# Kernel optimization log

Hardware: AMD Instinct MI355X
Metric: run time of the kernel (lower is better)

The kernel has to match this reference:

```python
import jax, jax.numpy as jnp
import numpy as np

SQRT2 = 1.4142135623730951  # ScaleCostWeight(sqrt(2)) applied to residuals
N_ITERS = 10
DAMP = 1e-8  # tiny Tikhonov for numerical safety of the 6x6 solve


def _hat(phi):
    x, y, z = phi[0], phi[1], phi[2]
    o = jnp.zeros((), phi.dtype)
    return jnp.stack([jnp.stack([o, -z, y]),
                      jnp.stack([z, o, -x]),
                      jnp.stack([-y, x, o])])


def se3_exp(xi):
    # xi: [6] = [rho (trans), phi (rot)] -> 4x4 SE3 matrix
    rho, phi = xi[:3], xi[3:]
    theta2 = jnp.sum(phi * phi)
    small = theta2 < 1e-12
    theta2s = jnp.where(small, 1.0, theta2)  # double-where for safe grads
    theta = jnp.sqrt(theta2s)
    A = jnp.where(small, 1.0, jnp.sin(theta) / theta)
    B = jnp.where(small, 0.5, (1.0 - jnp.cos(theta)) / theta2s)
    C = jnp.where(small, 1.0 / 6.0, (theta - jnp.sin(theta)) / (theta2s * theta))
    K = _hat(phi)
    K2 = K @ K
    I3 = jnp.eye(3, dtype=xi.dtype)
    R = I3 + A * K + B * K2
    V = I3 + B * K + C * K2
    t = V @ rho
    top = jnp.concatenate([R, t[:, None]], axis=1)
    bot = jnp.array([[0.0, 0.0, 0.0, 1.0]], dtype=xi.dtype)
    return jnp.concatenate([top, bot], axis=0)


def se3_inv(T):
    R = T[..., :3, :3]
    t = T[..., :3, 3:]
    Rt = jnp.swapaxes(R, -1, -2)
    top = jnp.concatenate([Rt, -(Rt @ t)], axis=-1)
    bot = jnp.broadcast_to(jnp.array([0.0, 0.0, 0.0, 1.0], T.dtype),
                           T.shape[:-2] + (1, 4))
    return jnp.concatenate([top, bot], axis=-2)


def _r_single(xi, T, src3, trg3, Wh, w):
    # residual of one batch element at local perturbation xi (retract on right)
    Tn = T @ se3_exp(xi)
    pred = Tn[:3, :3] @ src3 + Tn[:3, 3:4]          # [3, N]
    e = trg3 - pred                                  # [3, N]
    ew = jnp.einsum('nij,jn->in', Wh, e) * w         # cholesky-weighted, w: [1,N]
    return (ew * SQRT2).reshape(-1)                  # [3N]


def _forward(src4, trg4, w, T_init, inv_cov, T_s_v):
    src3 = src4[:, :3, :]
    trg3 = trg4[:, :3, :]
    # W_half = cholesky(inv_cov)^T, computed once (aux var, constant over iters)
    Wh = jnp.swapaxes(jnp.linalg.cholesky(inv_cov), -1, -2)  # [B, N, 3, 3]
    B = src4.shape[0]
    I6 = jnp.eye(6, dtype=src4.dtype)

    def step(T, _):
        xi0 = jnp.zeros((B, 6), T.dtype)
        J = jax.vmap(jax.jacfwd(_r_single), in_axes=(0, 0, 0, 0, 0, 0))(
            xi0, T, src3, trg3, Wh, w)               # [B, 3N, 6]
        r = jax.vmap(_r_single)(xi0, T, src3, trg3, Wh, w)  # [B, 3N]
        g = jnp.einsum('bri,br->bi', J, r)
        H = jnp.einsum('bri,brj->bij', J, J) + DAMP * I6
        dx = -jnp.linalg.solve(H, g[..., None])[..., 0]
        return T @ jax.vmap(se3_exp)(dx), None

    T, _ = jax.lax.scan(step, T_init, None, length=N_ITERS)
    T_sv = jnp.broadcast_to(T_s_v, (B, 4, 4))
    return se3_inv(T_sv) @ T @ T_sv


def setup_inputs() -> dict:
    key = jax.random.key(0)
    B, N = 256, 2048
    k1, k2, k3, k4, k5, k6 = jax.random.split(key, 6)
    src3 = 2.0 * jax.random.normal(k1, (B, 3, N), dtype=jnp.float32)
    # well-posed registration problem: trg = T_true * src + noise
    T_true = jax.vmap(se3_exp)(0.3 * jax.random.normal(k2, (B, 6), dtype=jnp.float32))
    trg3 = (jnp.einsum('bij,bjn->bin', T_true[:, :3, :3], src3)
            + T_true[:, :3, 3:4]
            + 0.01 * jax.random.normal(k3, (B, 3, N), dtype=jnp.float32))
    ones = jnp.ones((B, 1, N), dtype=jnp.float32)
    keypoints_3D_src = jnp.concatenate([src3, ones], axis=1)
    keypoints_3D_trg = jnp.concatenate([trg3, ones], axis=1)
    weights = jax.random.uniform(k4, (B, 1, N), dtype=jnp.float32,
                                 minval=0.1, maxval=1.0)
    A = 0.3 * jax.random.normal(k5, (B, N, 3, 3), dtype=jnp.float32)
    inv_cov_weights = A @ jnp.swapaxes(A, -1, -2) + jnp.eye(3, dtype=jnp.float32)
    T_trg_src_init = jax.vmap(se3_exp)(
        0.05 * jax.random.normal(k6, (B, 6), dtype=jnp.float32))
    T_s_v = se3_exp(jnp.array([0.1, -0.2, 0.3, 0.2, -0.1, 0.15], dtype=jnp.float32))
    return {"keypoints_3D_src": keypoints_3D_src,
            "keypoints_3D_trg": keypoints_3D_trg,
            "weights": weights,
            "T_trg_src_init": T_trg_src_init,
            "inv_cov_weights": inv_cov_weights,
            "T_s_v": T_s_v}


def reference(keypoints_3D_src, keypoints_3D_trg, weights, T_trg_src_init,
              inv_cov_weights, T_s_v):
    return _forward(keypoints_3D_src, keypoints_3D_trg, weights,
                    T_trg_src_init, inv_cov_weights, T_s_v)
```

## Files before the change

### kernel.cpp

```cpp
#include <hip/hip_runtime.h>
#include <math.h>

#define NPTS   2048
#define BD1    256
#define SPLIT  2
#define PPB    (NPTS / SPLIT)
#define PPT    (PPB / BD1)
#define NMOM   72
#define NITERS 10
#define DAMPF  1e-8f

__launch_bounds__(BD1, 1)
__global__ void moments_kernel(const float* __restrict__ src4,
                               const float* __restrict__ trg4,
                               const float* __restrict__ wts,
                               const float* __restrict__ icov,
                               float* __restrict__ mom, int B)
{
    const int b   = blockIdx.x >> 1;
    const int s   = blockIdx.x & 1;
    const int tid = threadIdx.x;

    const float* srcb = src4 + (size_t)b * 4 * NPTS;
    const float* trgb = trg4 + (size_t)b * 4 * NPTS;
    const float* wb   = wts  + (size_t)b * NPTS;
    const float* cb   = icov + (size_t)b * NPTS * 9;

    float acc[NMOM];
    #pragma unroll
    for (int k = 0; k < NMOM; ++k) acc[k] = 0.0f;

    #pragma unroll 2
    for (int kk = 0; kk < PPT; ++kk) {
        int n = s * PPB + kk * BD1 + tid;
        float sx = srcb[n], sy = srcb[NPTS + n], sz = srcb[2 * NPTS + n];
        float gx = trgb[n], gy = trgb[NPTS + n], gz = trgb[2 * NPTS + n];
        float w  = wb[n];
        const float* c = cb + (size_t)n * 9;
        float w2 = 2.0f * w * w;
        float W[6];
        W[0] = w2 * c[0];
        W[1] = w2 * c[3];
        W[2] = w2 * c[6];
        W[3] = w2 * c[4];
        W[4] = w2 * c[7];
        W[5] = w2 * c[8];

        float hx = W[0] * gx + W[1] * gy + W[2] * gz;
        float hy = W[1] * gx + W[3] * gy + W[4] * gz;
        float hz = W[2] * gx + W[4] * gy + W[5] * gz;

        float sv[3] = { sx, sy, sz };
        float hv[3] = { hx, hy, hz };
        float ss[6] = { sx*sx, sx*sy, sx*sz, sy*sy, sy*sz, sz*sz };

        #pragma unroll
        for (int ij = 0; ij < 6; ++ij) {
            acc[ij] += W[ij];
            #pragma unroll
            for (int c2 = 0; c2 < 3; ++c2) acc[6 + ij * 3 + c2] += W[ij] * sv[c2];
            #pragma unroll
            for (int cd = 0; cd < 6; ++cd) acc[24 + ij * 6 + cd] += W[ij] * ss[cd];
        }
        acc[60] += hx; acc[61] += hy; acc[62] += hz;
        #pragma unroll
        for (int c2 = 0; c2 < 3; ++c2)
            #pragma unroll
            for (int i = 0; i < 3; ++i) acc[63 + c2 * 3 + i] += sv[c2] * hv[i];
    }

    __shared__ float lds[36][BD1 + 1];
    #pragma unroll
    for (int h = 0; h < 2; ++h) {
        if (h) __syncthreads();
        #pragma unroll
        for (int k = 0; k < 36; ++k) lds[k][tid] = acc[h * 36 + k];
        __syncthreads();
        if (tid < 36) {
            const float* row = lds[tid];
            float s0 = 0.f, s1 = 0.f, s2 = 0.f, s3 = 0.f;
            #pragma unroll 8
            for (int j = 0; j < BD1; j += 4) {
                s0 += row[j]; s1 += row[j + 1]; s2 += row[j + 2]; s3 += row[j + 3];
            }
            mom[((size_t)s * NMOM + h * 36 + tid) * B + b] = (s0 + s1) + (s2 + s3);
        }
    }
}

__launch_bounds__(64, 1)
__global__ void solve_kernel(const float* __restrict__ mom,
                             const float* __restrict__ Tinit,
                             const float* __restrict__ Tsv,
                             float* __restrict__ out, int B)
{
    const int b = blockIdx.x * 64 + threadIdx.x;
    if (b >= B) return;

    float m[NMOM];
    #pragma unroll
    for (int k = 0; k < NMOM; ++k)
        m[k] = mom[k * B + b] + mom[(NMOM + k) * B + b];

    float Rm[3][3], tv[3];
    #pragma unroll
    for (int i = 0; i < 3; ++i) {
        #pragma unroll
        for (int j = 0; j < 3; ++j) Rm[i][j] = Tinit[b * 16 + i * 4 + j];
        tv[i] = Tinit[b * 16 + i * 4 + 3];
    }

    const int SY[3][3] = { {0,1,2}, {1,3,4}, {2,4,5} };

    for (int it = 0; it < NITERS; ++it) {
        float C1[6][3];
        #pragma unroll
        for (int ij = 0; ij < 6; ++ij) {
            float a0 = m[6 + ij * 3 + 0], a1 = m[6 + ij * 3 + 1], a2 = m[6 + ij * 3 + 2];
            #pragma unroll
            for (int a = 0; a < 3; ++a)
                C1[ij][a] = Rm[a][0] * a0 + Rm[a][1] * a1 + Rm[a][2] * a2;
        }
        float SM[3][3], SWp[3];
        #pragma unroll
        for (int i = 0; i < 3; ++i) {
            SM[i][0] = C1[SY[i][1]][2] - C1[SY[i][2]][1];
            SM[i][1] = C1[SY[i][2]][0] - C1[SY[i][0]][2];
            SM[i][2] = C1[SY[i][0]][1] - C1[SY[i][1]][0];
            SWp[i]   = C1[SY[i][0]][0] + C1[SY[i][1]][1] + C1[SY[i][2]][2];
        }
        float P2[6][6];
        #pragma unroll
        for (int ij = 0; ij < 6; ++ij) {
            float S00 = m[24 + ij * 6 + 0], S01 = m[24 + ij * 6 + 1], S02 = m[24 + ij * 6 + 2];
            float S11 = m[24 + ij * 6 + 3], S12 = m[24 + ij * 6 + 4], S22 = m[24 + ij * 6 + 5];
            float U[3][3];
            #pragma unroll
            for (int a = 0; a < 3; ++a) {
                U[a][0] = Rm[a][0] * S00 + Rm[a][1] * S01 + Rm[a][2] * S02;
                U[a][1] = Rm[a][0] * S01 + Rm[a][1] * S11 + Rm[a][2] * S12;
                U[a][2] = Rm[a][0] * S02 + Rm[a][1] * S12 + Rm[a][2] * S22;
            }
            P2[0][ij] = U[0][0]*Rm[0][0] + U[0][1]*Rm[0][1] + U[0][2]*Rm[0][2];
            P2[1][ij] = U[0][0]*Rm[1][0] + U[0][1]*Rm[1][1] + U[0][2]*Rm[1][2];
            P2[2][ij] = U[0][0]*Rm[2][0] + U[0][1]*Rm[2][1] + U[0][2]*Rm[2][2];
            P2[3][ij] = U[1][0]*Rm[1][0] + U[1][1]*Rm[1][1] + U[1][2]*Rm[1][2];
            P2[4][ij] = U[1][0]*Rm[2][0] + U[1][1]*Rm[2][1] + U[1][2]*Rm[2][2];
            P2[5][ij] = U[2][0]*Rm[2][0] + U[2][1]*Rm[2][1] + U[2][2]*Rm[2][2];
        }
        float SN00 = -P2[5][3] + 2.f * P2[4][4] - P2[3][5];
        float SN01 = -P2[2][4] + P2[5][1] + P2[1][5] - P2[4][2];
        float SN02 = -P2[4][1] + P2[2][3] + P2[3][2] - P2[1][4];
        float SN11 =  2.f * P2[2][2] - P2[5][0] - P2[0][5];
        float SN12 =  P2[4][0] - P2[2][1] - P2[1][2] + P2[0][4];
        float SN22 = -P2[3][0] + 2.f * P2[1][1] - P2[0][3];

        float SWt0 = m[0]*tv[0] + m[1]*tv[1] + m[2]*tv[2];
        float SWt1 = m[1]*tv[0] + m[3]*tv[1] + m[4]*tv[2];
        float SWt2 = m[2]*tv[0] + m[4]*tv[1] + m[5]*tv[2];
        float Su[3] = { m[60] - SWp[0] - SWt0,
                        m[61] - SWp[1] - SWt1,
                        m[62] - SWp[2] - SWt2 };

        float G[3][3];
        #pragma unroll
        for (int a = 0; a < 3; ++a)
            #pragma unroll
            for (int bb = 0; bb < 3; ++bb)
                G[a][bb] = Rm[a][0]*m[63 + 0 + bb] + Rm[a][1]*m[63 + 3 + bb] + Rm[a][2]*m[63 + 6 + bb];
        float ch[3] = { G[1][2] - G[2][1], G[2][0] - G[0][2], G[0][1] - G[1][0] };
        float pw[3];
        pw[0] = P2[1][2] + P2[3][4] + P2[4][5] - P2[2][1] - P2[4][3] - P2[5][4];
        pw[1] = P2[2][0] + P2[4][1] + P2[5][2] - P2[0][2] - P2[1][4] - P2[2][5];
        pw[2] = P2[0][1] + P2[1][3] + P2[2][4] - P2[1][0] - P2[3][1] - P2[4][2];
        float Sq[3];
        #pragma unroll
        for (int i = 0; i < 3; ++i)
            Sq[i] = ch[i] - pw[i] + SM[0][i]*tv[0] + SM[1][i]*tv[1] + SM[2][i]*tv[2];

        float Hm[6][6];
        Hm[0][0] = m[0]; Hm[0][1] = m[1]; Hm[0][2] = m[2];
        Hm[1][1] = m[3]; Hm[1][2] = m[4]; Hm[2][2] = m[5];
        #pragma unroll
        for (int i = 0; i < 3; ++i) {
            Hm[i][3] = -SM[i][0]; Hm[i][4] = -SM[i][1]; Hm[i][5] = -SM[i][2];
        }
        Hm[3][3] = -SN00; Hm[3][4] = -SN01; Hm[3][5] = -SN02;
        Hm[4][4] = -SN11; Hm[4][5] = -SN12; Hm[5][5] = -SN22;
        #pragma unroll
        for (int i = 0; i < 6; ++i) {
            Hm[i][i] += DAMPF;
            #pragma unroll
            for (int j = 0; j < 6; ++j)
                if (j < i) Hm[i][j] = Hm[j][i];
        }
        float rhs[6] = { Su[0], Su[1], Su[2], Sq[0], Sq[1], Sq[2] };

        float L[6][6];
        #pragma unroll
        for (int i = 0; i < 6; ++i) {
            #pragma unroll
            for (int j = 0; j < 6; ++j) {
                if (j > i) continue;
                float sum = Hm[i][j];
                #pragma unroll
                for (int k2 = 0; k2 < 6; ++k2)
                    if (k2 < j) sum -= L[i][k2] * L[j][k2];
                if (i == j) L[i][i] = sqrtf(sum);
                else        L[i][j] = sum / L[j][j];
            }
        }
        float z[6];
        #pragma unroll
        for (int i = 0; i < 6; ++i) {
            float sum = rhs[i];
            #pragma unroll
            for (int k2 = 0; k2 < 6; ++k2)
                if (k2 < i) sum -= L[i][k2] * z[k2];
            z[i] = sum / L[i][i];
        }
        float y[6];
        #pragma unroll
        for (int i = 5; i >= 0; --i) {
            float sum = z[i];
            #pragma unroll
            for (int k2 = 0; k2 < 6; ++k2)
                if (k2 > i) sum -= L[k2][i] * y[k2];
            y[i] = sum / L[i][i];
        }

        float drx = Rm[0][0]*y[0] + Rm[1][0]*y[1] + Rm[2][0]*y[2];
        float dry = Rm[0][1]*y[0] + Rm[1][1]*y[1] + Rm[2][1]*y[2];
        float drz = Rm[0][2]*y[0] + Rm[1][2]*y[1] + Rm[2][2]*y[2];
        float dpx = Rm[0][0]*y[3] + Rm[1][0]*y[4] + Rm[2][0]*y[5];
        float dpy = Rm[0][1]*y[3] + Rm[1][1]*y[4] + Rm[2][1]*y[5];
        float dpz = Rm[0][2]*y[3] + Rm[1][2]*y[4] + Rm[2][2]*y[5];

        float th2  = dpx*dpx + dpy*dpy + dpz*dpz;
        bool  sm   = th2 < 1e-12f;
        float th2s = sm ? 1.0f : th2;
        float th   = sqrtf(th2s);
        float sth  = sinf(th), cth = cosf(th);
        float Ae = sm ? 1.0f : sth / th;
        float Be = sm ? 0.5f : (1.0f - cth) / th2s;
        float Ce = sm ? (1.0f / 6.0f) : (th - sth) / (th2s * th);
        float Rd00 = 1.0f + Be * (dpx*dpx - th2);
        float Rd01 = -Ae * dpz + Be * dpx * dpy;
        float Rd02 =  Ae * dpy + Be * dpx * dpz;
        float Rd10 =  Ae * dpz + Be * dpx * dpy;
        float Rd11 = 1.0f + Be * (dpy*dpy - th2);
        float Rd12 = -Ae * dpx + Be * dpy * dpz;
        float Rd20 = -Ae * dpy + Be * dpx * dpz;
        float Rd21 =  Ae * dpx + Be * dpy * dpz;
        float Rd22 = 1.0f + Be * (dpz*dpz - th2);
        float V00 = 1.0f + Ce * (dpx*dpx - th2);
        float V01 = -Be * dpz + Ce * dpx * dpy;
        float V02 =  Be * dpy + Ce * dpx * dpz;
        float V10 =  Be * dpz + Ce * dpx * dpy;
        float V11 = 1.0f + Ce * (dpy*dpy - th2);
        float V12 = -Be * dpx + Ce * dpy * dpz;
        float V20 = -Be * dpy + Ce * dpx * dpz;
        float V21 =  Be * dpx + Ce * dpy * dpz;
        float V22 = 1.0f + Ce * (dpz*dpz - th2);
        float tdx = V00 * drx + V01 * dry + V02 * drz;
        float tdy = V10 * drx + V11 * dry + V12 * drz;
        float tdz = V20 * drx + V21 * dry + V22 * drz;

        float nR[3][3];
        nR[0][0] = Rm[0][0]*Rd00 + Rm[0][1]*Rd10 + Rm[0][2]*Rd20;
        nR[0][1] = Rm[0][0]*Rd01 + Rm[0][1]*Rd11 + Rm[0][2]*Rd21;
        nR[0][2] = Rm[0][0]*Rd02 + Rm[0][1]*Rd12 + Rm[0][2]*Rd22;
        nR[1][0] = Rm[1][0]*Rd00 + Rm[1][1]*Rd10 + Rm[1][2]*Rd20;
        nR[1][1] = Rm[1][0]*Rd01 + Rm[1][1]*Rd11 + Rm[1][2]*Rd21;
        nR[1][2] = Rm[1][0]*Rd02 + Rm[1][1]*Rd12 + Rm[1][2]*Rd22;
        nR[2][0] = Rm[2][0]*Rd00 + Rm[2][1]*Rd10 + Rm[2][2]*Rd20;
        nR[2][1] = Rm[2][0]*Rd01 + Rm[2][1]*Rd11 + Rm[2][2]*Rd21;
        nR[2][2] = Rm[2][0]*Rd02 + Rm[2][1]*Rd12 + Rm[2][2]*Rd22;
        float ntx = Rm[0][0]*tdx + Rm[0][1]*tdy + Rm[0][2]*tdz + tv[0];
        float nty = Rm[1][0]*tdx + Rm[1][1]*tdy + Rm[1][2]*tdz + tv[1];
        float ntz = Rm[2][0]*tdx + Rm[2][1]*tdy + Rm[2][2]*tdz + tv[2];
        #pragma unroll
        for (int i = 0; i < 3; ++i)
            #pragma unroll
            for (int j = 0; j < 3; ++j) Rm[i][j] = nR[i][j];
        tv[0] = ntx; tv[1] = nty; tv[2] = ntz;
    }

    {
        float R00 = Rm[0][0], R01 = Rm[0][1], R02 = Rm[0][2];
        float R10 = Rm[1][0], R11 = Rm[1][1], R12 = Rm[1][2];
        float R20 = Rm[2][0], R21 = Rm[2][1], R22 = Rm[2][2];
        float tx = tv[0], ty = tv[1], tz = tv[2];

        float Rv00 = Tsv[0], Rv01 = Tsv[1], Rv02 = Tsv[2],  tvx = Tsv[3];
        float Rv10 = Tsv[4], Rv11 = Tsv[5], Rv12 = Tsv[6],  tvy = Tsv[7];
        float Rv20 = Tsv[8], Rv21 = Tsv[9], Rv22 = Tsv[10], tvz = Tsv[11];

        float P00 = R00*Rv00 + R01*Rv10 + R02*Rv20;
        float P01 = R00*Rv01 + R01*Rv11 + R02*Rv21;
        float P02 = R00*Rv02 + R01*Rv12 + R02*Rv22;
        float P10 = R10*Rv00 + R11*Rv10 + R12*Rv20;
        float P11 = R10*Rv01 + R11*Rv11 + R12*Rv21;
        float P12 = R10*Rv02 + R11*Rv12 + R12*Rv22;
        float P20 = R20*Rv00 + R21*Rv10 + R22*Rv20;
        float P21 = R20*Rv01 + R21*Rv11 + R22*Rv21;
        float P22 = R20*Rv02 + R21*Rv12 + R22*Rv22;
        float Ptx = R00*tvx + R01*tvy + R02*tvz + tx;
        float Pty = R10*tvx + R11*tvy + R12*tvz + ty;
        float Ptz = R20*tvx + R21*tvy + R22*tvz + tz;

        float ex = Ptx - tvx, ey = Pty - tvy, ez = Ptz - tvz;
        float* o = out + (size_t)b * 16;
        o[0]  = Rv00*P00 + Rv10*P10 + Rv20*P20;
        o[1]  = Rv00*P01 + Rv10*P11 + Rv20*P21;
        o[2]  = Rv00*P02 + Rv10*P12 + Rv20*P22;
        o[3]  = Rv00*ex  + Rv10*ey  + Rv20*ez;
        o[4]  = Rv01*P00 + Rv11*P10 + Rv21*P20;
        o[5]  = Rv01*P01 + Rv11*P11 + Rv21*P21;
        o[6]  = Rv01*P02 + Rv11*P12 + Rv21*P22;
        o[7]  = Rv01*ex  + Rv11*ey  + Rv21*ez;
        o[8]  = Rv02*P00 + Rv12*P10 + Rv22*P20;
        o[9]  = Rv02*P01 + Rv12*P11 + Rv22*P21;
        o[10] = Rv02*P02 + Rv12*P12 + Rv22*P22;
        o[11] = Rv02*ex  + Rv12*ey  + Rv22*ez;
        o[12] = 0.0f; o[13] = 0.0f; o[14] = 0.0f; o[15] = 1.0f;
    }
}

extern "C" void kernel_launch(void* const* d_in, const int* in_sizes, int n_in,
                              void* d_out, int out_size, void* d_ws, size_t ws_size,
                              hipStream_t stream)
{
    const float* src4  = (const float*)d_in[0];
    const float* trg4  = (const float*)d_in[1];
    const float* wts   = (const float*)d_in[2];
    const float* Tinit = (const float*)d_in[3];
    const float* icov  = (const float*)d_in[4];
    const float* Tsv   = (const float*)d_in[5];

    const int B = in_sizes[3] / 16;
    float* mom = (float*)d_ws;

    hipLaunchKernelGGL(moments_kernel, dim3(B * SPLIT), dim3(BD1), 0, stream,
                       src4, trg4, wts, icov, mom, B);
    hipLaunchKernelGGL(solve_kernel, dim3((B + 63) / 64), dim3(64), 0, stream,
                       mom, Tinit, Tsv, (float*)d_out, B);
}
```

Measured before the change: 110.1 us.

## Stage inverse covariances through LDS with coalesced float4 loads and split points four ways

```diff
diff --git a/kernel.cpp b/kernel.cpp
--- a/kernel.cpp
+++ b/kernel.cpp
@@ -3,40 +3,60 @@
 
 #define NPTS   2048
 #define BD1    256
-#define SPLIT  2
+#define SPLIT  4
 #define PPB    (NPTS / SPLIT)
-#define PPT    (PPB / BD1)
+#define TILE   256
+#define NTILE  (PPB / TILE)
 #define NMOM   72
 #define NITERS 10
 #define DAMPF  1e-8f
 
-__launch_bounds__(BD1, 1)
+__launch_bounds__(BD1, 3)
 __global__ void moments_kernel(const float* __restrict__ src4,
                                const float* __restrict__ trg4,
                                const float* __restrict__ wts,
                                const float* __restrict__ icov,
                                float* __restrict__ mom, int B)
 {
-    const int b   = blockIdx.x >> 1;
-    const int s   = blockIdx.x & 1;
+    const int b   = blockIdx.x / SPLIT;
+    const int s   = blockIdx.x % SPLIT;
     const int tid = threadIdx.x;
 
     const float* srcb = src4 + (size_t)b * 4 * NPTS;
     const float* trgb = trg4 + (size_t)b * 4 * NPTS;
     const float* wb   = wts  + (size_t)b * NPTS;
-    const float* cb   = icov + (size_t)b * NPTS * 9;
+    const float* cb   = icov + ((size_t)b * NPTS + (size_t)s * PPB) * 9;
+
+    __shared__ float ic[TILE * 9];
+    __shared__ float lds[36][BD1 + 1];
 
     float acc[NMOM];
     #pragma unroll
     for (int k = 0; k < NMOM; ++k) acc[k] = 0.0f;
 
-    #pragma unroll 2
-    for (int kk = 0; kk < PPT; ++kk) {
-        int n = s * PPB + kk * BD1 + tid;
-        float sx = srcb[n], sy = srcb[NPTS + n], sz = srcb[2 * NPTS + n];
-        float gx = trgb[n], gy = trgb[NPTS + n], gz = trgb[2 * NPTS + n];
-        float w  = wb[n];
-        const float* c = cb + (size_t)n * 9;
+    #pragma unroll
+    for (int tile = 0; tile < NTILE; ++tile) {
+        const int n = tile * TILE + tid;
+        const int ng = s * PPB + n;
+
+        const float4* g4 = (const float4*)(cb + (size_t)tile * TILE * 9);
+        float4 v0 = g4[tid];
+        float4 v1 = g4[tid + 256];
+        float4 v2;
+        if (tid < 64) v2 = g4[tid + 512];
+
+        float sx = srcb[ng], sy = srcb[NPTS + ng], sz = srcb[2 * NPTS + ng];
+        float gx = trgb[ng], gy = trgb[NPTS + ng], gz = trgb[2 * NPTS + ng];
+        float w  = wb[ng];
+
+        if (tile) __syncthreads();
+        float4* l4 = (float4*)ic;
+        l4[tid]       = v0;
+        l4[tid + 256] = v1;
+        if (tid < 64) l4[tid + 512] = v2;
+        __syncthreads();
+
+        const float* c = ic + tid * 9;
         float w2 = 2.0f * w * w;
         float W[6];
         W[0] = w2 * c[0];
@@ -69,10 +89,9 @@
             for (int i = 0; i < 3; ++i) acc[63 + c2 * 3 + i] += sv[c2] * hv[i];
     }
 
-    __shared__ float lds[36][BD1 + 1];
     #pragma unroll
     for (int h = 0; h < 2; ++h) {
-        if (h) __syncthreads();
+        __syncthreads();
         #pragma unroll
         for (int k = 0; k < 36; ++k) lds[k][tid] = acc[h * 36 + k];
         __syncthreads();
@@ -99,8 +118,13 @@
 
     float m[NMOM];
     #pragma unroll
-    for (int k = 0; k < NMOM; ++k)
-        m[k] = mom[k * B + b] + mom[(NMOM + k) * B + b];
+    for (int k = 0; k < NMOM; ++k) {
+        float v = 0.0f;
+        #pragma unroll
+        for (int s = 0; s < SPLIT; ++s)
+            v += mom[((size_t)s * NMOM + k) * B + b];
+        m[k] = v;
+    }
 
     float Rm[3][3], tv[3];
     #pragma unroll
```

Result: slower. 115.6 us (+5.0%).
